# Kernel optimization log

Measured on AMD Instinct MI355X. Metric: run time of the kernel, lower is better.

The kernel has to match this reference:

```python
import jax, jax.numpy as jnp
from jax import lax
import numpy as np

H, W, C_IN, C_OUT, K, GROUPS, EPS = 1024, 1024, 64, 128, 3, 32, 1e-5


def setup_inputs() -> dict:
    key = jax.random.key(0)
    k = jax.random.split(key, 7)
    # flax Conv default kernel init (lecun_normal) scale approximated; exact init values
    # don't matter for a correctness baseline, only shapes/math.
    x = jax.random.normal(k[0], (H, W, C_IN), dtype=jnp.float32)
    W1 = jax.random.normal(k[1], (K, K, C_IN, C_OUT), dtype=jnp.float32) * (1.0 / np.sqrt(K * K * C_IN))
    b1 = jnp.zeros((C_OUT,), dtype=jnp.float32)
    W2 = jax.random.normal(k[2], (1, 1, C_IN, C_OUT), dtype=jnp.float32) * (1.0 / np.sqrt(C_IN))
    b2 = jnp.zeros((C_OUT,), dtype=jnp.float32)
    gn_scale = jnp.ones((C_OUT,), dtype=jnp.float32)
    gn_bias = jnp.zeros((C_OUT,), dtype=jnp.float32)
    return {"x": x, "W1": W1, "b1": b1, "W2": W2, "b2": b2,
            "gn_scale": gn_scale, "gn_bias": gn_bias}


def _forward(x, W1, b1, W2, b2, gn_scale, gn_bias):
    nx, ny = x.shape[0], x.shape[1]
    # NOTE: linspace spans [0, nx] inclusive (one past last valid index nx-1),
    # matching the original; map_coordinates order=1 zero-fills out of range.
    coords = jnp.meshgrid(jnp.linspace(0, nx, nx // 2), jnp.linspace(0, ny, ny // 2))
    x = jax.vmap(jax.scipy.ndimage.map_coordinates, in_axes=(-1, None, None), out_axes=-1)(x, coords, 1)
    # dual conv (SAME padding, stride 1), unbatched -> add/remove batch dim
    xb = x[None]  # [1, h, w, C_IN]
    dn = ('NHWC', 'HWIO', 'NHWC')
    y1 = lax.conv_general_dilated(xb, W1, (1, 1), 'SAME', dimension_numbers=dn) + b1
    y2 = lax.conv_general_dilated(xb, W2, (1, 1), 'SAME', dimension_numbers=dn) + b2
    y = (y1 + y2)[0]  # [h, w, C_OUT]
    # GroupNorm (flax default: 32 groups, eps=1e-5, scale+bias)
    h, w, c = y.shape
    yg = y.reshape(h, w, GROUPS, c // GROUPS)
    mu = yg.mean(axis=(0, 1, 3), keepdims=True)
    var = yg.var(axis=(0, 1, 3), keepdims=True)
    yn = ((yg - mu) * lax.rsqrt(var + EPS)).reshape(h, w, c)
    return jax.nn.gelu(yn * gn_scale + gn_bias)  # flax gelu: approximate=True


def reference(x, W1, b1, W2, b2, gn_scale, gn_bias):
    return _forward(x, W1, b1, W2, b2, gn_scale, gn_bias)
```

## Files before the change

kernel.cpp:

```cpp
#include <hip/hip_runtime.h>
#include <math.h>

#define HI 1024
#define WI 1024
#define HO 512
#define WO 512
#define CIN 64
#define COUT 128
#define NW (9*CIN*COUT)

typedef __attribute__((ext_vector_type(8))) short bf16x8;
typedef __attribute__((ext_vector_type(4))) float f32x4;


#define GLDS(g, l) __builtin_amdgcn_global_load_lds( \
    (const __attribute__((address_space(1))) void*)(g), \
    (__attribute__((address_space(3))) void*)(l), 16, 0, 0)

__device__ __forceinline__ unsigned short f2bf(float f) {
    unsigned u = __float_as_uint(f);
    u += 0x7fffu + ((u >> 16) & 1u);
    return (unsigned short)(u >> 16);
}

__global__ void k_pack(const float* __restrict__ W1, const float* __restrict__ b1,
                       const float* __restrict__ W2, const float* __restrict__ b2,
                       unsigned short* __restrict__ Bpk, float* __restrict__ bf,
                       unsigned short* __restrict__ zeroz) {
    int idx = blockIdx.x * 256 + threadIdx.x;
    if (idx < NW) {
        int j  = idx & 7;
        int l  = (idx >> 3) & 63;
        int nf = (idx >> 9) & 7;
        int h  = (idx >> 12) & 1;
        int t  = idx >> 13;
        int cin  = (h << 5) + ((l >> 4) << 3) + j;
        int cout = (nf << 4) + (l & 15);
        float v = W1[(t * 64 + cin) * 128 + cout];
        if (t == 4) v += W2[cin * 128 + cout];
        Bpk[idx] = f2bf(v);
    } else if (idx < NW + COUT) {
        int c = idx - NW;
        bf[c] = b1[c] + b2[c];
    } else if (idx < NW + COUT + 64) {
        zeroz[idx - NW - COUT] = 0;
    }
}

__global__ void k_down(const float* __restrict__ x, unsigned short* __restrict__ xd) {
    int t = blockIdx.x * 256 + threadIdx.x;
    int c8 = t & 7;
    int j  = (t >> 3) & (WO - 1);
    int i  = t >> 12;
    const float step = 1024.0f / 511.0f;
    float tr = (float)j * step;
    float tc = (float)i * step;
    int r0 = (int)tr; float fr = tr - (float)r0;
    int c0 = (int)tc; float fc = tc - (float)c0;
    float w00 = (1.f - fr) * (1.f - fc);
    float w01 = (1.f - fr) * fc;
    float w10 = fr * (1.f - fc);
    float w11 = fr * fc;
    float a0 = 0.f, a1 = 0.f, a2 = 0.f, a3 = 0.f;
    float a4 = 0.f, a5 = 0.f, a6 = 0.f, a7 = 0.f;
    const float* xb = x + (c8 << 3);
    #define TAP(R, C, W) \
        if ((R) < HI && (C) < WI) { \
            const float* p = xb + ((((R) << 10) + (C)) << 6); \
            float4 v0 = *(const float4*)p; \
            float4 v1 = *(const float4*)(p + 4); \
            a0 += (W) * v0.x; a1 += (W) * v0.y; a2 += (W) * v0.z; a3 += (W) * v0.w; \
            a4 += (W) * v1.x; a5 += (W) * v1.y; a6 += (W) * v1.z; a7 += (W) * v1.w; \
        }
    TAP(r0,     c0,     w00)
    TAP(r0,     c0 + 1, w01)
    TAP(r0 + 1, c0,     w10)
    TAP(r0 + 1, c0 + 1, w11)
    #undef TAP
    uint4 pk;
    pk.x = (unsigned)f2bf(a0) | ((unsigned)f2bf(a1) << 16);
    pk.y = (unsigned)f2bf(a2) | ((unsigned)f2bf(a3) << 16);
    pk.z = (unsigned)f2bf(a4) | ((unsigned)f2bf(a5) << 16);
    pk.w = (unsigned)f2bf(a6) | ((unsigned)f2bf(a7) << 16);
    *(uint4*)&xd[(((i << 9) + j) << 6) + (c8 << 3)] = pk;
}

__global__ __launch_bounds__(512, 2) void k_conv(
        const unsigned short* __restrict__ xd,
        const unsigned short* __restrict__ Bpk,
        const float* __restrict__ bf,
        const unsigned short* __restrict__ zeroz,
        unsigned short* __restrict__ yb, float* __restrict__ part) {
    __shared__ short lxs[2][324 * 64];
    __shared__ float sred[8][32];

    const int tid = threadIdx.x;
    const int l   = tid & 63;
    const int w   = tid >> 6;
    const int trow = blockIdx.x >> 3;
    const int tcq  = blockIdx.x & 7;
    const int gr0  = trow << 4;
    const int gc0b = (tcq << 2) << 4;

    const int wq  = w & 3;
    const int wh  = w >> 2;
    const int qg  = l >> 4;
    const int p15 = l & 15;
    const int wr0 = (wq >> 1) << 3;
    const int wc0 = (wq & 1) << 3;
    const int colbase = wc0 + (l & 7);
    int rowbase[4];
    #pragma unroll
    for (int mf = 0; mf < 4; ++mf)
        rowbase[mf] = (wr0 + 2 * mf + (p15 >> 3)) * 18 + colbase;

    const bf16x8* Bbase = (const bf16x8*)Bpk;
    bf16x8 b0[4];
    #pragma unroll
    for (int nf = 0; nf < 4; ++nf)
        b0[nf] = Bbase[(((wh << 2) + nf) << 6) + l];
    f32x4 bias4 = *(const f32x4*)&bf[(wh << 6) + (qg << 2)];

    auto STAGE = [&](int bufi, int gc0t) {
        #pragma unroll
        for (int k = 0; k < 6; ++k) {
            int idx = tid + (k << 9);
            if (idx < 324 * 8) {
                int pos = idx >> 3, c = idx & 7;
                int row = (pos * 57) >> 10;
                int col = pos - row * 18;
                int gr = gr0 + row - 1, gc = gc0t + col - 1;
                bool inpx = (gr >= 0) && (gr < HO) && (gc >= 0) && (gc < WO);
                const unsigned short* src = inpx
                    ? xd + (((gr << 9) + gc) << 6) + ((c ^ (col & 7)) << 3)
                    : zeroz;
                GLDS(src, (char*)lxs[bufi] + (((w << 6) + (k << 9)) << 4));
            }
        }
    };

    float s[4], s2[4];
    #pragma unroll
    for (int nf = 0; nf < 4; ++nf) { s[nf] = 0.f; s2[nf] = 0.f; }

    STAGE(0, gc0b);
    __syncthreads();

    #pragma unroll 1
    for (int t = 0; t < 4; ++t) {
        if (t < 3) STAGE((t + 1) & 1, gc0b + ((t + 1) << 4));

        const char* lx = (const char*)lxs[t & 1];
        const int gc0 = gc0b + (t << 4);

        f32x4 acc[4][4];
        #pragma unroll
        for (int nf = 0; nf < 4; ++nf) {
            #pragma unroll
            for (int mf = 0; mf < 4; ++mf)
                acc[mf][nf] = bias4;
        }

        bf16x8 bcur[4];
        #pragma unroll
        for (int nf = 0; nf < 4; ++nf) bcur[nf] = b0[nf];

        #pragma unroll 1
        for (int th = 0; th < 18; ++th) {
            const int thn = (th < 17) ? th + 1 : 0;
            bf16x8 bnxt[4];
            {
                const bf16x8* Bth = Bbase + (thn << 9);
                #pragma unroll
                for (int nf = 0; nf < 4; ++nf)
                    bnxt[nf] = Bth[(((wh << 2) + nf) << 6) + l];
            }
            const int tt = th >> 1;
            const int h  = th & 1;
            const int dy = (tt * 11) >> 5;
            const int dx = tt - dy * 3;
            const int chunkx = ((h << 2) + qg) ^ ((colbase + dx) & 7);
            bf16x8 a[4];
            #pragma unroll
            for (int mf = 0; mf < 4; ++mf)
                a[mf] = *(const bf16x8*)(lx +
                         (rowbase[mf] + dy * 18 + dx) * 128 + (chunkx << 4));
            #pragma unroll
            for (int mf = 0; mf < 4; ++mf) {
                #pragma unroll
                for (int nf = 0; nf < 4; ++nf)
                    acc[mf][nf] = __builtin_amdgcn_mfma_f32_16x16x32_bf16(
                        bcur[nf], a[mf], acc[mf][nf], 0, 0, 0);
            }
            #pragma unroll
            for (int nf = 0; nf < 4; ++nf)
                bcur[nf] = bnxt[nf];
        }

        #pragma unroll
        for (int mf = 0; mf < 4; ++mf) {
            int gr = gr0 + wr0 + (mf << 1) + (p15 >> 3);
            int gc = gc0 + wc0 + (p15 & 7);
            unsigned short* op = yb + (((gr << 9) + gc) << 7) + (wh << 6) + (qg << 2);
            #pragma unroll
            for (int nf = 0; nf < 4; ++nf) {
                f32x4 v = acc[mf][nf];
                ushort4 o;
                o.x = f2bf(v[0]); o.y = f2bf(v[1]); o.z = f2bf(v[2]); o.w = f2bf(v[3]);
                *(ushort4*)(op + (nf << 4)) = o;
                s[nf]  += v[0] + v[1] + v[2] + v[3];
                s2[nf] += v[0] * v[0] + v[1] * v[1] + v[2] * v[2] + v[3] * v[3];
            }
        }

        __syncthreads();
    }

    #pragma unroll
    for (int nf = 0; nf < 4; ++nf) {
        s[nf]  += __shfl_xor(s[nf], 1);  s[nf]  += __shfl_xor(s[nf], 2);
        s[nf]  += __shfl_xor(s[nf], 4);  s[nf]  += __shfl_xor(s[nf], 8);
        s2[nf] += __shfl_xor(s2[nf], 1); s2[nf] += __shfl_xor(s2[nf], 2);
        s2[nf] += __shfl_xor(s2[nf], 4); s2[nf] += __shfl_xor(s2[nf], 8);
    }
    if (p15 == 0) {
        #pragma unroll
        for (int nf = 0; nf < 4; ++nf) {
            sred[w][(nf << 2) + qg]      = s[nf];
            sred[w][16 + (nf << 2) + qg] = s2[nf];
        }
    }
    __syncthreads();
    if (tid < 64) {
        int isS2 = tid >> 5;
        int g    = tid & 31;
        int gh   = g >> 4;
        int g16  = (g & 15) + (isS2 << 4);
        float v = sred[(gh << 2) + 0][g16] + sred[(gh << 2) + 1][g16]
                + sred[(gh << 2) + 2][g16] + sred[(gh << 2) + 3][g16];
        part[(blockIdx.x << 6) + (isS2 << 5) + g] = v;
    }
}

__global__ void k_final(const float* __restrict__ part, float* __restrict__ params) {
    __shared__ float sh[256];
    int t = threadIdx.x;
    int col = t & 63, q = t >> 6;
    float s = 0.f;
    for (int r = q; r < 256; r += 4) s += part[r * 64 + col];
    sh[t] = s;
    __syncthreads();
    if (t < 64) sh[t] = sh[t] + sh[64 + t] + sh[128 + t] + sh[192 + t];
    __syncthreads();
    if (t < 32) {
        const float invN = 1.0f / (512.0f * 512.0f * 4.0f);
        float mu  = sh[t] * invN;
        float var = sh[32 + t] * invN - mu * mu;
        params[t]      = mu;
        params[32 + t] = rsqrtf(var + 1e-5f);
    }
}

__global__ void k_gelu(const unsigned short* __restrict__ yb, float* __restrict__ out,
                       const float* __restrict__ params, const float* __restrict__ scale,
                       const float* __restrict__ bias) {
    int t = blockIdx.x * 256 + threadIdx.x;
    int c0 = (t & 15) << 3;
    uint4 raw = ((const uint4*)yb)[t];
    unsigned us[8];
    us[0] = raw.x & 0xffffu; us[1] = raw.x >> 16;
    us[2] = raw.y & 0xffffu; us[3] = raw.y >> 16;
    us[4] = raw.z & 0xffffu; us[5] = raw.z >> 16;
    us[6] = raw.w & 0xffffu; us[7] = raw.w >> 16;
    int g0 = c0 >> 2;
    float mu0 = params[g0],     iv0 = params[32 + g0];
    float mu1 = params[g0 + 1], iv1 = params[33 + g0];
    float scb[8], bib[8];
    *(float4*)&scb[0] = *(const float4*)&scale[c0];
    *(float4*)&scb[4] = *(const float4*)&scale[c0 + 4];
    *(float4*)&bib[0] = *(const float4*)&bias[c0];
    *(float4*)&bib[4] = *(const float4*)&bias[c0 + 4];
    float o[8];
    #pragma unroll
    for (int k = 0; k < 8; ++k) {
        float xf = __uint_as_float(us[k] << 16);
        float mu = (k < 4) ? mu0 : mu1;
        float iv = (k < 4) ? iv0 : iv1;
        float z  = (xf - mu) * iv * scb[k] + bib[k];
        float a  = 0.7978845608028654f * (z + 0.044715f * z * z * z);
        o[k] = z / (1.0f + __expf(-2.0f * a));
    }
    float4* op = (float4*)(out + ((size_t)t << 3));
    op[0] = make_float4(o[0], o[1], o[2], o[3]);
    op[1] = make_float4(o[4], o[5], o[6], o[7]);
}

extern "C" void kernel_launch(void* const* d_in, const int* in_sizes, int n_in,
                              void* d_out, int out_size, void* d_ws, size_t ws_size,
                              hipStream_t stream) {
    const float* x  = (const float*)d_in[0];
    const float* W1 = (const float*)d_in[1];
    const float* b1 = (const float*)d_in[2];
    const float* W2 = (const float*)d_in[3];
    const float* b2 = (const float*)d_in[4];
    const float* gs = (const float*)d_in[5];
    const float* gb = (const float*)d_in[6];
    float* out = (float*)d_out;

    char* ws = (char*)d_ws;
    unsigned short* xd    = (unsigned short*)d_out;
    unsigned short* yb    = (unsigned short*)(ws);
    unsigned short* Bpk   = (unsigned short*)(ws + 67108864);
    float* bf             = (float*)(ws + 67256320);
    float* part           = (float*)(ws + 67256832);
    float* params         = (float*)(ws + 67518976);
    unsigned short* zeroz = (unsigned short*)(ws + 67519232);

    k_pack<<<(NW + COUT + 64 + 255) / 256, 256, 0, stream>>>(W1, b1, W2, b2, Bpk, bf, zeroz);
    k_down<<<(HO * WO * (CIN / 8)) / 256, 256, 0, stream>>>(x, xd);
    k_conv<<<256, 512, 0, stream>>>(xd, Bpk, bf, zeroz, yb, part);
    k_final<<<1, 256, 0, stream>>>(part, params);
    k_gelu<<<(HO * WO * COUT / 8) / 256, 256, 0, stream>>>(yb, out, params, gs, gb);
}
```

Measured before the change: 180.9 us.

## Fuse conv, GroupNorm stats and GELU via grid barrier; merge prep kernels

Merges the weight-pack and bilinear-downsample kernels into one launch. The conv kernel then absorbs the stats finalisation and the GELU pass. After writing its partial sums, each block joins a software grid barrier built on an atomic counter. Every block then reduces all partials itself and normalises and activates its own output tile, while that tile's bf16 data may still be in cache. This removes launch gaps and a separate pass, but relies on all 256 blocks being co-resident, and runs the bandwidth-bound elementwise phase with fewer threads in flight.

```diff
diff --git a/kernel.cpp b/kernel.cpp
--- a/kernel.cpp
+++ b/kernel.cpp
@@ -23,76 +23,85 @@
     return (unsigned short)(u >> 16);
 }
 
-__global__ void k_pack(const float* __restrict__ W1, const float* __restrict__ b1,
+__global__ void k_prep(const float* __restrict__ x,
+                       const float* __restrict__ W1, const float* __restrict__ b1,
                        const float* __restrict__ W2, const float* __restrict__ b2,
+                       unsigned short* __restrict__ xd,
                        unsigned short* __restrict__ Bpk, float* __restrict__ bf,
-                       unsigned short* __restrict__ zeroz) {
-    int idx = blockIdx.x * 256 + threadIdx.x;
-    if (idx < NW) {
-        int j  = idx & 7;
-        int l  = (idx >> 3) & 63;
-        int nf = (idx >> 9) & 7;
-        int h  = (idx >> 12) & 1;
-        int t  = idx >> 13;
-        int cin  = (h << 5) + ((l >> 4) << 3) + j;
-        int cout = (nf << 4) + (l & 15);
-        float v = W1[(t * 64 + cin) * 128 + cout];
-        if (t == 4) v += W2[cin * 128 + cout];
-        Bpk[idx] = f2bf(v);
-    } else if (idx < NW + COUT) {
-        int c = idx - NW;
-        bf[c] = b1[c] + b2[c];
-    } else if (idx < NW + COUT + 64) {
-        zeroz[idx - NW - COUT] = 0;
+                       unsigned short* __restrict__ zeroz, unsigned* __restrict__ ctr) {
+    int bid = blockIdx.x;
+    if (bid < 8192) {
+        int t = bid * 256 + threadIdx.x;
+        int c8 = t & 7;
+        int j  = (t >> 3) & (WO - 1);
+        int i  = t >> 12;
+        const float step = 1024.0f / 511.0f;
+        float tr = (float)j * step;
+        float tc = (float)i * step;
+        int r0 = (int)tr; float fr = tr - (float)r0;
+        int c0 = (int)tc; float fc = tc - (float)c0;
+        float w00 = (1.f - fr) * (1.f - fc);
+        float w01 = (1.f - fr) * fc;
+        float w10 = fr * (1.f - fc);
+        float w11 = fr * fc;
+        float a0 = 0.f, a1 = 0.f, a2 = 0.f, a3 = 0.f;
+        float a4 = 0.f, a5 = 0.f, a6 = 0.f, a7 = 0.f;
+        const float* xb = x + (c8 << 3);
+        #define TAP(R, C, W) \
+            if ((R) < HI && (C) < WI) { \
+                const float* p = xb + ((((R) << 10) + (C)) << 6); \
+                float4 v0 = *(const float4*)p; \
+                float4 v1 = *(const float4*)(p + 4); \
+                a0 += (W) * v0.x; a1 += (W) * v0.y; a2 += (W) * v0.z; a3 += (W) * v0.w; \
+                a4 += (W) * v1.x; a5 += (W) * v1.y; a6 += (W) * v1.z; a7 += (W) * v1.w; \
+            }
+        TAP(r0,     c0,     w00)
+        TAP(r0,     c0 + 1, w01)
+        TAP(r0 + 1, c0,     w10)
+        TAP(r0 + 1, c0 + 1, w11)
+        #undef TAP
+        uint4 pk;
+        pk.x = (unsigned)f2bf(a0) | ((unsigned)f2bf(a1) << 16);
+        pk.y = (unsigned)f2bf(a2) | ((unsigned)f2bf(a3) << 16);
+        pk.z = (unsigned)f2bf(a4) | ((unsigned)f2bf(a5) << 16);
+        pk.w = (unsigned)f2bf(a6) | ((unsigned)f2bf(a7) << 16);
+        *(uint4*)&xd[(((i << 9) + j) << 6) + (c8 << 3)] = pk;
+    } else {
+        int idx = (bid - 8192) * 256 + threadIdx.x;
+        if (idx < NW) {
+            int j  = idx & 7;
+            int l  = (idx >> 3) & 63;
+            int nf = (idx >> 9) & 7;
+            int h  = (idx >> 12) & 1;
+            int t  = idx >> 13;
+            int cin  = (h << 5) + ((l >> 4) << 3) + j;
+            int cout = (nf << 4) + (l & 15);
+            float v = W1[(t * 64 + cin) * 128 + cout];
+            if (t == 4) v += W2[cin * 128 + cout];
+            Bpk[idx] = f2bf(v);
+        } else if (idx < NW + COUT) {
+            int c = idx - NW;
+            bf[c] = b1[c] + b2[c];
+        } else if (idx < NW + COUT + 64) {
+            zeroz[idx - NW - COUT] = 0;
+        } else if (idx == NW + COUT + 64) {
+            *ctr = 0;
+        }
     }
 }
 
-__global__ void k_down(const float* __restrict__ x, unsigned short* __restrict__ xd) {
-    int t = blockIdx.x * 256 + threadIdx.x;
-    int c8 = t & 7;
-    int j  = (t >> 3) & (WO - 1);
-    int i  = t >> 12;
-    const float step = 1024.0f / 511.0f;
-    float tr = (float)j * step;
-    float tc = (float)i * step;
-    int r0 = (int)tr; float fr = tr - (float)r0;
-    int c0 = (int)tc; float fc = tc - (float)c0;
-    float w00 = (1.f - fr) * (1.f - fc);
-    float w01 = (1.f - fr) * fc;
-    float w10 = fr * (1.f - fc);
-    float w11 = fr * fc;
-    float a0 = 0.f, a1 = 0.f, a2 = 0.f, a3 = 0.f;
-    float a4 = 0.f, a5 = 0.f, a6 = 0.f, a7 = 0.f;
-    const float* xb = x + (c8 << 3);
-    #define TAP(R, C, W) \
-        if ((R) < HI && (C) < WI) { \
-            const float* p = xb + ((((R) << 10) + (C)) << 6); \
-            float4 v0 = *(const float4*)p; \
-            float4 v1 = *(const float4*)(p + 4); \
-            a0 += (W) * v0.x; a1 += (W) * v0.y; a2 += (W) * v0.z; a3 += (W) * v0.w; \
-            a4 += (W) * v1.x; a5 += (W) * v1.y; a6 += (W) * v1.z; a7 += (W) * v1.w; \
-        }
-    TAP(r0,     c0,     w00)
-    TAP(r0,     c0 + 1, w01)
-    TAP(r0 + 1, c0,     w10)
-    TAP(r0 + 1, c0 + 1, w11)
-    #undef TAP
-    uint4 pk;
-    pk.x = (unsigned)f2bf(a0) | ((unsigned)f2bf(a1) << 16);
-    pk.y = (unsigned)f2bf(a2) | ((unsigned)f2bf(a3) << 16);
-    pk.z = (unsigned)f2bf(a4) | ((unsigned)f2bf(a5) << 16);
-    pk.w = (unsigned)f2bf(a6) | ((unsigned)f2bf(a7) << 16);
-    *(uint4*)&xd[(((i << 9) + j) << 6) + (c8 << 3)] = pk;
-}
-
-__global__ __launch_bounds__(512, 2) void k_conv(
+__global__ __launch_bounds__(512, 2) void k_fused(
         const unsigned short* __restrict__ xd,
         const unsigned short* __restrict__ Bpk,
         const float* __restrict__ bf,
         const unsigned short* __restrict__ zeroz,
-        unsigned short* __restrict__ yb, float* __restrict__ part) {
+        unsigned short* __restrict__ yb, float* part, unsigned* ctr,
+        const float* __restrict__ gscale, const float* __restrict__ gbias,
+        float* __restrict__ out) {
     __shared__ short lxs[2][324 * 64];
     __shared__ float sred[8][32];
+    __shared__ float fin[256];
+    __shared__ float pl[64];
 
     const int tid = threadIdx.x;
     const int l   = tid & 63;
@@ -240,59 +249,72 @@
                 + sred[(gh << 2) + 2][g16] + sred[(gh << 2) + 3][g16];
         part[(blockIdx.x << 6) + (isS2 << 5) + g] = v;
     }
-}
-
-__global__ void k_final(const float* __restrict__ part, float* __restrict__ params) {
-    __shared__ float sh[256];
-    int t = threadIdx.x;
-    int col = t & 63, q = t >> 6;
-    float s = 0.f;
-    for (int r = q; r < 256; r += 4) s += part[r * 64 + col];
-    sh[t] = s;
-    __syncthreads();
-    if (t < 64) sh[t] = sh[t] + sh[64 + t] + sh[128 + t] + sh[192 + t];
-    __syncthreads();
-    if (t < 32) {
+
+    __threadfence();
+    __syncthreads();
+    if (tid == 0) {
+        atomicAdd(ctr, 1u);
+        while (__hip_atomic_load(ctr, __ATOMIC_ACQUIRE, __HIP_MEMORY_SCOPE_AGENT) < 256u)
+            __builtin_amdgcn_s_sleep(2);
+    }
+    __syncthreads();
+
+    if (tid < 256) {
+        int col = tid & 63, q = tid >> 6;
+        float ps = 0.f;
+        for (int r = q; r < 256; r += 4)
+            ps += __hip_atomic_load(&part[r * 64 + col], __ATOMIC_RELAXED,
+                                    __HIP_MEMORY_SCOPE_AGENT);
+        fin[tid] = ps;
+    }
+    __syncthreads();
+    if (tid < 64) fin[tid] = fin[tid] + fin[64 + tid] + fin[128 + tid] + fin[192 + tid];
+    __syncthreads();
+    if (tid < 32) {
         const float invN = 1.0f / (512.0f * 512.0f * 4.0f);
-        float mu  = sh[t] * invN;
-        float var = sh[32 + t] * invN - mu * mu;
-        params[t]      = mu;
-        params[32 + t] = rsqrtf(var + 1e-5f);
-    }
-}
-
-__global__ void k_gelu(const unsigned short* __restrict__ yb, float* __restrict__ out,
-                       const float* __restrict__ params, const float* __restrict__ scale,
-                       const float* __restrict__ bias) {
-    int t = blockIdx.x * 256 + threadIdx.x;
-    int c0 = (t & 15) << 3;
-    uint4 raw = ((const uint4*)yb)[t];
-    unsigned us[8];
-    us[0] = raw.x & 0xffffu; us[1] = raw.x >> 16;
-    us[2] = raw.y & 0xffffu; us[3] = raw.y >> 16;
-    us[4] = raw.z & 0xffffu; us[5] = raw.z >> 16;
-    us[6] = raw.w & 0xffffu; us[7] = raw.w >> 16;
-    int g0 = c0 >> 2;
-    float mu0 = params[g0],     iv0 = params[32 + g0];
-    float mu1 = params[g0 + 1], iv1 = params[33 + g0];
-    float scb[8], bib[8];
-    *(float4*)&scb[0] = *(const float4*)&scale[c0];
-    *(float4*)&scb[4] = *(const float4*)&scale[c0 + 4];
-    *(float4*)&bib[0] = *(const float4*)&bias[c0];
-    *(float4*)&bib[4] = *(const float4*)&bias[c0 + 4];
-    float o[8];
-    #pragma unroll
-    for (int k = 0; k < 8; ++k) {
-        float xf = __uint_as_float(us[k] << 16);
-        float mu = (k < 4) ? mu0 : mu1;
-        float iv = (k < 4) ? iv0 : iv1;
-        float z  = (xf - mu) * iv * scb[k] + bib[k];
-        float a  = 0.7978845608028654f * (z + 0.044715f * z * z * z);
-        o[k] = z / (1.0f + __expf(-2.0f * a));
-    }
-    float4* op = (float4*)(out + ((size_t)t << 3));
-    op[0] = make_float4(o[0], o[1], o[2], o[3]);
-    op[1] = make_float4(o[4], o[5], o[6], o[7]);
+        float mu  = fin[tid] * invN;
+        float var = fin[32 + tid] * invN - mu * mu;
+        pl[tid]      = mu;
+        pl[32 + tid] = rsqrtf(var + 1e-5f);
+    }
+    __syncthreads();
+
+    #pragma unroll 1
+    for (int it = tid; it < 16384; it += 512) {
+        int q  = it & 15;
+        int px = it >> 4;
+        int gc = gc0b + (px & 63);
+        int gr = gr0 + (px >> 6);
+        size_t base = ((((size_t)gr << 9) + gc) << 7) + (q << 3);
+        uint4 raw = *(const uint4*)&yb[base];
+        unsigned us[8];
+        us[0] = raw.x & 0xffffu; us[1] = raw.x >> 16;
+        us[2] = raw.y & 0xffffu; us[3] = raw.y >> 16;
+        us[4] = raw.z & 0xffffu; us[5] = raw.z >> 16;
+        us[6] = raw.w & 0xffffu; us[7] = raw.w >> 16;
+        int c0 = q << 3;
+        int g0 = c0 >> 2;
+        float mu0 = pl[g0],     iv0 = pl[32 + g0];
+        float mu1 = pl[g0 + 1], iv1 = pl[33 + g0];
+        float scb[8], bib[8];
+        *(float4*)&scb[0] = *(const float4*)&gscale[c0];
+        *(float4*)&scb[4] = *(const float4*)&gscale[c0 + 4];
+        *(float4*)&bib[0] = *(const float4*)&gbias[c0];
+        *(float4*)&bib[4] = *(const float4*)&gbias[c0 + 4];
+        float o[8];
+        #pragma unroll
+        for (int k = 0; k < 8; ++k) {
+            float xf = __uint_as_float(us[k] << 16);
+            float mu = (k < 4) ? mu0 : mu1;
+            float iv = (k < 4) ? iv0 : iv1;
+            float z  = (xf - mu) * iv * scb[k] + bib[k];
+            float a  = 0.7978845608028654f * (z + 0.044715f * z * z * z);
+            o[k] = z / (1.0f + __expf(-2.0f * a));
+        }
+        float4* op = (float4*)(out + base);
+        op[0] = make_float4(o[0], o[1], o[2], o[3]);
+        op[1] = make_float4(o[4], o[5], o[6], o[7]);
+    }
 }
 
 extern "C" void kernel_launch(void* const* d_in, const int* in_sizes, int n_in,
@@ -313,12 +335,9 @@
     unsigned short* Bpk   = (unsigned short*)(ws + 67108864);
     float* bf             = (float*)(ws + 67256320);
     float* part           = (float*)(ws + 67256832);
-    float* params         = (float*)(ws + 67518976);
     unsigned short* zeroz = (unsigned short*)(ws + 67519232);
-
-    k_pack<<<(NW + COUT + 64 + 255) / 256, 256, 0, stream>>>(W1, b1, W2, b2, Bpk, bf, zeroz);
-    k_down<<<(HO * WO * (CIN / 8)) / 256, 256, 0, stream>>>(x, xd);
-    k_conv<<<256, 512, 0, stream>>>(xd, Bpk, bf, zeroz, yb, part);
-    k_final<<<1, 256, 0, stream>>>(part, params);
-    k_gelu<<<(HO * WO * COUT / 8) / 256, 256, 0, stream>>>(yb, out, params, gs, gb);
+    unsigned* ctr         = (unsigned*)(ws + 67519360);
+
+    k_prep<<<8192 + 289, 256, 0, stream>>>(x, W1, b1, W2, b2, xd, Bpk, bf, zeroz, ctr);
+    k_fused<<<256, 512, 0, stream>>>(xd, Bpk, bf, zeroz, yb, part, ctr, gs, gb, out);
 }
```

After: 215.7 us. +19.2%, slower.
